# Kernel optimization log

Measured on AMD Instinct MI355X. Metric: run time of the kernel, lower is better.

Reference implementation:

```python
import jax, jax.numpy as jnp
import numpy as np


def rotary_pos_emb(x):
    # x: [..., seq, dim], dim even. Interleaved (GPT-NeoX-style pairwise) rotary.
    dim, seq = x.shape[-1], x.shape[-2]
    ts = jnp.arange(0, dim, 2, dtype=jnp.float32)
    inv_freqs = 10000.0 ** (-ts / dim)
    grid = jnp.arange(seq, dtype=jnp.float32)[:, None] * inv_freqs[None, :]  # [s, dim//2]
    sin = jnp.repeat(jnp.sin(grid), 2, axis=-1).astype(x.dtype)  # [s, dim]
    cos = jnp.repeat(jnp.cos(grid), 2, axis=-1).astype(x.dtype)  # [s, dim]
    x1, x2 = x[..., ::2], x[..., 1::2]
    xs = jnp.stack([-x2, x1], axis=-1).reshape(x.shape)  # interleave (-x2, x1)
    return x * cos + xs * sin


def setup_inputs() -> dict:
    key = jax.random.key(0)
    kx, kq, kk, kv, ko = jax.random.split(key, 5)
    B, S, D = 2, 2048, 1024
    scale = 1.0 / np.sqrt(D)
    x = jax.random.normal(kx, (B, S, D), dtype=jnp.float32)
    mask = jnp.tril(jnp.ones((S, S), dtype=bool))  # causal
    Wq = jax.random.normal(kq, (D, D), dtype=jnp.float32) * scale
    Wk = jax.random.normal(kk, (D, D), dtype=jnp.float32) * scale
    Wv = jax.random.normal(kv, (D, D), dtype=jnp.float32) * scale
    Wo = jax.random.normal(ko, (D, D), dtype=jnp.float32) * scale
    return {"x": x, "mask": mask, "Wq": Wq, "Wk": Wk, "Wv": Wv, "Wo": Wo}


def reference(x, mask, Wq, Wk, Wv, Wo):
    H = 16
    POS_PORTION = 0.5
    B, S, D = x.shape
    K = D // H
    p = int(K * POS_PORTION)

    q = (x @ Wq) / (K ** 0.5)
    q = q.reshape(B, S, H, K).transpose(0, 2, 1, 3)  # b h l k
    q = jnp.concatenate([rotary_pos_emb(q[..., :p]), q[..., p:]], axis=-1)

    k = (x @ Wk).reshape(B, S, H, K).transpose(0, 2, 1, 3)
    k = jnp.concatenate([rotary_pos_emb(k[..., :p]), k[..., p:]], axis=-1)

    v = (x @ Wv).reshape(B, S, H, K).transpose(0, 2, 1, 3)

    logits = jnp.einsum('bhik,bhjk->bhij', q, k)
    # full-precision masked softmax
    l32 = logits.astype(jnp.float32)
    l32 = jnp.where(mask, l32, -1e30)
    a = jax.nn.softmax(l32, axis=-1).astype(logits.dtype)

    y = jnp.einsum('bhij,bhjv->bhiv', a, v)
    y = y.transpose(0, 2, 1, 3).reshape(B, S, D)  # b l (h v)
    return y @ Wo
```

## Files before the change

### kernel.cpp

```cpp
#include <hip/hip_runtime.h>
#include <cstdint>
#include <cstddef>

typedef __bf16 bf16;
typedef __bf16 bf16x8 __attribute__((ext_vector_type(8)));
typedef float  f32x4  __attribute__((ext_vector_type(4)));

#define B_  2
#define S_  2048
#define D_  1024
#define H_  16
#define KH  64

__device__ __forceinline__ void gload_lds16(const bf16* gp, bf16* lds_base) {
    __builtin_amdgcn_global_load_lds(
        (const __attribute__((address_space(1))) unsigned int*)gp,
        (__attribute__((address_space(3))) unsigned int*)lds_base,
        16, 0, 0);
}

__global__ __launch_bounds__(256) void prep(
    const float* __restrict__ x, bf16* __restrict__ xb,
    const float* __restrict__ Wq, const float* __restrict__ Wk,
    const float* __restrict__ Wv, const float* __restrict__ Wo,
    bf16* __restrict__ WqkvT, bf16* __restrict__ WoT)
{
    __shared__ bf16 tl[64][72];
    int z = blockIdx.x;
    if (z < 4096) {
        const int i = (z * 256 + threadIdx.x) * 4;
        const float4 v = *(const float4*)(x + i);
        union { int2 w; bf16 e[4]; } u;
        u.e[0] = (bf16)v.x; u.e[1] = (bf16)v.y;
        u.e[2] = (bf16)v.z; u.e[3] = (bf16)v.w;
        *(int2*)(xb + i) = u.w;
        return;
    }
    z -= 4096;
    const int zx = z & 15, zy = (z >> 4) & 15, zw = z >> 8;
    const float* src = (zw == 0) ? Wq : (zw == 1) ? Wk : (zw == 2) ? Wv : Wo;
    bf16* dst = (zw < 3) ? (WqkvT + (size_t)zw * D_ * D_) : WoT;
    const int r0 = zy * 64;
    const int c0 = zx * 64;
    const int t  = threadIdx.x;
    {
        const int r = t >> 2, cs = (t & 3) * 16;
        const float4* p = (const float4*)(src + (size_t)(r0 + r) * D_ + c0 + cs);
        float4 a0 = p[0], a1 = p[1], a2 = p[2], a3 = p[3];
        tl[cs +  0][r] = (bf16)a0.x; tl[cs +  1][r] = (bf16)a0.y;
        tl[cs +  2][r] = (bf16)a0.z; tl[cs +  3][r] = (bf16)a0.w;
        tl[cs +  4][r] = (bf16)a1.x; tl[cs +  5][r] = (bf16)a1.y;
        tl[cs +  6][r] = (bf16)a1.z; tl[cs +  7][r] = (bf16)a1.w;
        tl[cs +  8][r] = (bf16)a2.x; tl[cs +  9][r] = (bf16)a2.y;
        tl[cs + 10][r] = (bf16)a2.z; tl[cs + 11][r] = (bf16)a2.w;
        tl[cs + 12][r] = (bf16)a3.x; tl[cs + 13][r] = (bf16)a3.y;
        tl[cs + 14][r] = (bf16)a3.z; tl[cs + 15][r] = (bf16)a3.w;
    }
    __syncthreads();
    {
        const int c = t >> 2, rs = (t & 3) * 16;
        union { int4 v[2]; bf16 e[16]; } u;
#pragma unroll
        for (int i = 0; i < 16; ++i) u.e[i] = tl[c][rs + i];
        int4* p = (int4*)(dst + (size_t)(c0 + c) * D_ + r0 + rs);
        p[0] = u.v[0]; p[1] = u.v[1];
    }
}

template <int EPI, int BN>
__global__ __launch_bounds__(256, 2) void gemm_bt(
    const bf16* __restrict__ A, const bf16* __restrict__ BT,
    float* __restrict__ C, int N, int Kd,
    bf16* __restrict__ qp, bf16* __restrict__ kp, bf16* __restrict__ vp)
{
    constexpr int NJF = BN / 32;
    __shared__ bf16 As[128 * 64];
    __shared__ bf16 Bs[BN * 64];
    const int tid  = threadIdx.x;
    const int lane = tid & 63;
    const int wave = tid >> 6;
    const int l15  = lane & 15;
    const int quad = lane >> 4;
    const int m0 = blockIdx.y * 128;
    const int n0 = blockIdx.x * BN;
    const int wm = (wave >> 1) * 64;
    const int wn = (wave & 1) * (BN / 2);

    f32x4 acc[4][NJF];
#pragma unroll
    for (int i = 0; i < 4; ++i)
#pragma unroll
        for (int j = 0; j < NJF; ++j) acc[i][j] = f32x4{0.f, 0.f, 0.f, 0.f};

    for (int k0 = 0; k0 < Kd; k0 += 64) {
        __syncthreads();
#pragma unroll
        for (int c = 0; c < 4; ++c) {
            const int base  = wave * 4096 + c * 1024;
            const int flatb = base + lane * 16;
            const int row   = flatb >> 7;
            const int col   = (flatb & 127) >> 1;
            gload_lds16(A + (size_t)(m0 + row) * Kd + k0 + col, As + (base >> 1));
        }
#pragma unroll
        for (int c = 0; c < NJF; ++c) {
            const int base  = wave * (BN * 32) + c * 1024;
            const int flatb = base + lane * 16;
            const int row   = flatb >> 7;
            const int col   = (flatb & 127) >> 1;
            gload_lds16(BT + (size_t)(n0 + row) * Kd + k0 + col, Bs + (base >> 1));
        }
        __syncthreads();
#pragma unroll
        for (int kk = 0; kk < 64; kk += 32) {
            bf16x8 af[4], bfv[NJF];
#pragma unroll
            for (int i = 0; i < 4; ++i)
                af[i] = *(const bf16x8*)&As[(wm + i * 16 + l15) * 64 + kk + quad * 8];
#pragma unroll
            for (int j = 0; j < NJF; ++j)
                bfv[j] = *(const bf16x8*)&Bs[(wn + j * 16 + l15) * 64 + kk + quad * 8];
#pragma unroll
            for (int i = 0; i < 4; ++i)
#pragma unroll
                for (int j = 0; j < NJF; ++j)
                    acc[i][j] = __builtin_amdgcn_mfma_f32_16x16x32_bf16(
                        af[i], bfv[j], acc[i][j], 0, 0, 0);
        }
    }

#pragma unroll
    for (int i = 0; i < 4; ++i)
#pragma unroll
        for (int j = 0; j < NJF; ++j) {
            const int Rb = m0 + wm + i * 16 + quad * 4;
            const int Cc = n0 + wn + j * 16 + l15;
            if (EPI == 0) {
#pragma unroll
                for (int r = 0; r < 4; ++r)
                    C[(size_t)(Rb + r) * N + Cc] = acc[i][j][r];
            } else {
                const int sec = Cc >> 10, cc = Cc & 1023;
                const int h = cc >> 6, kd = cc & 63;
#pragma unroll
                for (int r = 0; r < 4; ++r) {
                    const int row = Rb + r;
                    const int b = row >> 11, s = row & (S_ - 1);
                    float v = acc[i][j][r];
                    if (sec == 0) {
                        qp[((size_t)(b * H_ + h) * S_ + s) * KH + kd] =
                            (bf16)(v * 0.1803368801111204f);
                    } else if (sec == 1) {
                        if ((kd >> 4) < 2) {
                            const float partner = __shfl_xor(v, 1);
                            const float inv = __builtin_exp2f(
                                -(float)(kd >> 1) * (13.28771237954945f / 16.f));
                            const float ang = (float)s * inv;
                            float sn, cn;
                            __sincosf(ang, &sn, &cn);
                            v = (l15 & 1) ? fmaf(partner, sn, v * cn)
                                          : fmaf(-partner, sn, v * cn);
                        }
                        kp[((size_t)(b * H_ + h) * S_ + s) * KH + kd] = (bf16)v;
                    } else {
                        vp[((size_t)(b * H_ + h) * KH + kd) * S_ + s] = (bf16)v;
                    }
                }
            }
        }
}

__global__ __launch_bounds__(128, 2) void attn(
    const bf16* __restrict__ q, const bf16* __restrict__ k,
    const bf16* __restrict__ vt, bf16* __restrict__ y)
{
    __shared__ bf16 Ks[2][64 * 64];
    __shared__ bf16 VTs[2][64 * 64];
    __shared__ bf16 Ps[2][2][16][64];

    const int z  = blockIdx.x;
    const int v_ = z & 7;
    const int u_ = (z >> 3) & 31;
    const int w_ = z >> 8;
    const int bh = u_;
    const int qt = (w_ == 0) ? v_ : (w_ == 1) ? (15 - v_)
                 : (w_ == 2) ? (16 + v_) : (31 - v_);
    const int b  = bh >> 4, h = bh & 15;
    const int t    = threadIdx.x;
    const int lane = t & 63, wave = t >> 6;
    const int l15  = lane & 15, quad = lane >> 4;
    const int wrow = qt * 64 + wave * 32;

    const bf16* kbh = k  + (size_t)bh * S_ * KH;
    const bf16* vbh = vt + (size_t)bh * KH * S_;

    const int srow = lane >> 3;
    const int sg   = (lane & 7) ^ srow;

    auto stage = [&](int jt, int bb) {
        const int j0 = jt * 64;
#pragma unroll
        for (int i = 0; i < 4; ++i) {
            const int c = wave * 4 + i;
            gload_lds16(kbh + (size_t)(j0 + c * 8 + srow) * KH + sg * 8,
                        &Ks[bb][c * 8 * 64]);
            gload_lds16(vbh + (size_t)(c * 8 + srow) * S_ + j0 + sg * 8,
                        &VTs[bb][c * 8 * 64]);
        }
    };

    bf16x8 qf[2][2];
#pragma unroll
    for (int mi = 0; mi < 2; ++mi) {
        const bf16* qp = q + ((size_t)bh * S_ + wrow + mi * 16 + l15) * KH + quad * 8;
        qf[mi][0] = *(const bf16x8*)qp;
        qf[mi][1] = *(const bf16x8*)(qp + 32);
        const float s = (float)(wrow + mi * 16 + l15);
#pragma unroll
        for (int tt = 0; tt < 4; ++tt) {
            const int i = quad * 4 + tt;
            const float inv = exp2f(-(float)i * (13.28771237954945f / 16.f));
            const float ang = s * inv;
            const float sn = sinf(ang), cn = cosf(ang);
            const float x0 = (float)qf[mi][0][2 * tt], x1 = (float)qf[mi][0][2 * tt + 1];
            qf[mi][0][2 * tt]     = (bf16)(x0 * cn - x1 * sn);
            qf[mi][0][2 * tt + 1] = (bf16)(x1 * cn + x0 * sn);
        }
    }

    bf16x8 ones;
#pragma unroll
    for (int i = 0; i < 8; ++i) ones[i] = (bf16)1.0f;

    f32x4 accO[2][4], lacc[2];
#pragma unroll
    for (int mi = 0; mi < 2; ++mi) {
#pragma unroll
        for (int j = 0; j < 4; ++j) accO[mi][j] = f32x4{0.f, 0.f, 0.f, 0.f};
        lacc[mi] = f32x4{0.f, 0.f, 0.f, 0.f};
    }

    const int nj = qt + 1;
    stage(0, 0);
    for (int jt = 0; jt < nj; ++jt) {
        const int bb = jt & 1;
        __syncthreads();
        if (jt + 1 < nj) stage(jt + 1, bb ^ 1);

        f32x4 accS[2][4];
#pragma unroll
        for (int mi = 0; mi < 2; ++mi)
#pragma unroll
            for (int nb = 0; nb < 4; ++nb) accS[mi][nb] = f32x4{0.f, 0.f, 0.f, 0.f};
#pragma unroll
        for (int c = 0; c < 2; ++c) {
            bf16x8 kf[4];
#pragma unroll
            for (int nb = 0; nb < 4; ++nb)
                kf[nb] = *(const bf16x8*)
                    &Ks[bb][(nb * 16 + l15) * 64 + (((c * 4 + quad) ^ (l15 & 7)) * 8)];
#pragma unroll
            for (int mi = 0; mi < 2; ++mi)
#pragma unroll
                for (int nb = 0; nb < 4; ++nb)
                    accS[mi][nb] = __builtin_amdgcn_mfma_f32_16x16x32_bf16(
                        qf[mi][c], kf[nb], accS[mi][nb], 0, 0, 0);
        }

        if (jt == nj - 1) {
            const int j0 = jt * 64;
#pragma unroll
            for (int mi = 0; mi < 2; ++mi)
#pragma unroll
                for (int nb = 0; nb < 4; ++nb)
#pragma unroll
                    for (int r = 0; r < 4; ++r) {
                        const int qi = wrow + mi * 16 + quad * 4 + r;
                        const int ki = j0 + nb * 16 + l15;
                        if (ki > qi) accS[mi][nb][r] = -1e30f;
                    }
        }

#pragma unroll
        for (int mi = 0; mi < 2; ++mi)
#pragma unroll
            for (int nb = 0; nb < 4; ++nb)
#pragma unroll
                for (int r = 0; r < 4; ++r) {
                    const float p = __builtin_amdgcn_exp2f(accS[mi][nb][r]);
                    const int row = quad * 4 + r;
                    Ps[wave][mi][row][(((nb * 2 + (l15 >> 3)) ^ (row & 7)) * 8) + (l15 & 7)]
                        = (bf16)p;
                }

#pragma unroll
        for (int c = 0; c < 2; ++c) {
            bf16x8 vf[4];
#pragma unroll
            for (int vb = 0; vb < 4; ++vb)
                vf[vb] = *(const bf16x8*)
                    &VTs[bb][(vb * 16 + l15) * 64 + (((c * 4 + quad) ^ (l15 & 7)) * 8)];
            bf16x8 pf[2];
#pragma unroll
            for (int mi = 0; mi < 2; ++mi)
                pf[mi] = *(const bf16x8*)
                    &Ps[wave][mi][l15][((c * 4 + quad) ^ (l15 & 7)) * 8];
#pragma unroll
            for (int mi = 0; mi < 2; ++mi) {
#pragma unroll
                for (int vb = 0; vb < 4; ++vb)
                    accO[mi][vb] = __builtin_amdgcn_mfma_f32_16x16x32_bf16(
                        pf[mi], vf[vb], accO[mi][vb], 0, 0, 0);
                lacc[mi] = __builtin_amdgcn_mfma_f32_16x16x32_bf16(
                    pf[mi], ones, lacc[mi], 0, 0, 0);
            }
        }
    }

#pragma unroll
    for (int mi = 0; mi < 2; ++mi) {
        float rinv[4];
#pragma unroll
        for (int r = 0; r < 4; ++r) rinv[r] = 1.0f / lacc[mi][r];
#pragma unroll
        for (int vb = 0; vb < 4; ++vb)
#pragma unroll
            for (int r = 0; r < 4; ++r) {
                const int row = wrow + mi * 16 + quad * 4 + r;
                const int col = h * KH + vb * 16 + l15;
                y[((size_t)b * S_ + row) * D_ + col] = (bf16)(accO[mi][vb][r] * rinv[r]);
            }
    }
}

extern "C" void kernel_launch(void* const* d_in, const int* in_sizes, int n_in,
                              void* d_out, int out_size, void* d_ws, size_t ws_size,
                              hipStream_t stream)
{
    (void)in_sizes; (void)n_in; (void)out_size; (void)ws_size;
    const float* x  = (const float*)d_in[0];
    const float* Wq = (const float*)d_in[2];
    const float* Wk = (const float*)d_in[3];
    const float* Wv = (const float*)d_in[4];
    const float* Wo = (const float*)d_in[5];
    float* out = (float*)d_out;

    char* ws = (char*)d_ws;
    bf16* WqkvT = (bf16*)(ws + 0);
    bf16* WoT   = (bf16*)(ws + 6291456);
    bf16* xb    = (bf16*)(ws + 8388608);
    bf16* qw    = (bf16*)(ws + 16777216);
    bf16* kw    = (bf16*)(ws + 25165824);
    bf16* vtw   = (bf16*)(ws + 33554432);
    bf16* yw    = (bf16*)(ws + 41943040);

    hipLaunchKernelGGL(prep, dim3(5120), dim3(256), 0, stream,
                       x, xb, Wq, Wk, Wv, Wo, WqkvT, WoT);
    hipLaunchKernelGGL((gemm_bt<1, 128>), dim3(24, 32), dim3(256), 0, stream,
                       xb, WqkvT, (float*)nullptr, 3072, 1024, qw, kw, vtw);
    hipLaunchKernelGGL(attn, dim3(1024), dim3(128), 0, stream, qw, kw, vtw, yw);
    hipLaunchKernelGGL((gemm_bt<0, 64>), dim3(16, 32), dim3(256), 0, stream,
                       yw, WoT, out, 1024, 1024,
                       (bf16*)nullptr, (bf16*)nullptr, (bf16*)nullptr);
}
```

Measured before the change: 204.8 us.

## Keep softmax probabilities in registers by computing transposed S tile

Swaps the MFMA operands for QK^T so each lane holds a column of S matching the A-operand layout of a 16x16x16 bf16 MFMA. The exponentiated probabilities then feed the PV product straight from registers, removing the per-wave LDS round trip for P. PV switches to the K=16 MFMA, which issues twice as many instructions. It also wraps the MFMA blocks in s_setprio to favour matrix issue. The causal mask indices are remapped to the transposed layout.

```diff
diff --git a/kernel.cpp b/kernel.cpp
--- a/kernel.cpp
+++ b/kernel.cpp
@@ -5,6 +5,7 @@
 typedef __bf16 bf16;
 typedef __bf16 bf16x8 __attribute__((ext_vector_type(8)));
 typedef float  f32x4  __attribute__((ext_vector_type(4)));
+typedef short  s16x4  __attribute__((ext_vector_type(4)));
 
 #define B_  2
 #define S_  2048
@@ -176,7 +177,6 @@
 {
     __shared__ bf16 Ks[2][64 * 64];
     __shared__ bf16 VTs[2][64 * 64];
-    __shared__ bf16 Ps[2][2][16][64];
 
     const int z  = blockIdx.x;
     const int v_ = z & 7;
@@ -228,9 +228,9 @@
         }
     }
 
-    bf16x8 ones;
-#pragma unroll
-    for (int i = 0; i < 8; ++i) ones[i] = (bf16)1.0f;
+    s16x4 ones4;
+#pragma unroll
+    for (int i = 0; i < 4; ++i) ones4[i] = (short)0x3F80;
 
     f32x4 accO[2][4], lacc[2];
 #pragma unroll
@@ -259,12 +259,14 @@
             for (int nb = 0; nb < 4; ++nb)
                 kf[nb] = *(const bf16x8*)
                     &Ks[bb][(nb * 16 + l15) * 64 + (((c * 4 + quad) ^ (l15 & 7)) * 8)];
+            __builtin_amdgcn_s_setprio(1);
 #pragma unroll
             for (int mi = 0; mi < 2; ++mi)
 #pragma unroll
                 for (int nb = 0; nb < 4; ++nb)
                     accS[mi][nb] = __builtin_amdgcn_mfma_f32_16x16x32_bf16(
-                        qf[mi][c], kf[nb], accS[mi][nb], 0, 0, 0);
+                        kf[nb], qf[mi][c], accS[mi][nb], 0, 0, 0);
+            __builtin_amdgcn_s_setprio(0);
         }
 
         if (jt == nj - 1) {
@@ -275,45 +277,43 @@
                 for (int nb = 0; nb < 4; ++nb)
 #pragma unroll
                     for (int r = 0; r < 4; ++r) {
-                        const int qi = wrow + mi * 16 + quad * 4 + r;
-                        const int ki = j0 + nb * 16 + l15;
+                        const int qi = wrow + mi * 16 + l15;
+                        const int ki = j0 + nb * 16 + quad * 4 + r;
                         if (ki > qi) accS[mi][nb][r] = -1e30f;
                     }
         }
 
+        s16x4 pf[2][4];
 #pragma unroll
         for (int mi = 0; mi < 2; ++mi)
 #pragma unroll
-            for (int nb = 0; nb < 4; ++nb)
-#pragma unroll
-                for (int r = 0; r < 4; ++r) {
-                    const float p = __builtin_amdgcn_exp2f(accS[mi][nb][r]);
-                    const int row = quad * 4 + r;
-                    Ps[wave][mi][row][(((nb * 2 + (l15 >> 3)) ^ (row & 7)) * 8) + (l15 & 7)]
-                        = (bf16)p;
-                }
-
-#pragma unroll
-        for (int c = 0; c < 2; ++c) {
-            bf16x8 vf[4];
+            for (int nb = 0; nb < 4; ++nb) {
+                union { bf16 hh[4]; s16x4 ss; } u;
+#pragma unroll
+                for (int r = 0; r < 4; ++r)
+                    u.hh[r] = (bf16)__builtin_amdgcn_exp2f(accS[mi][nb][r]);
+                pf[mi][nb] = u.ss;
+            }
+
+#pragma unroll
+        for (int nb = 0; nb < 4; ++nb) {
+            s16x4 vf[4];
 #pragma unroll
             for (int vb = 0; vb < 4; ++vb)
-                vf[vb] = *(const bf16x8*)
-                    &VTs[bb][(vb * 16 + l15) * 64 + (((c * 4 + quad) ^ (l15 & 7)) * 8)];
-            bf16x8 pf[2];
-#pragma unroll
-            for (int mi = 0; mi < 2; ++mi)
-                pf[mi] = *(const bf16x8*)
-                    &Ps[wave][mi][l15][((c * 4 + quad) ^ (l15 & 7)) * 8];
+                vf[vb] = *(const s16x4*)
+                    &VTs[bb][(vb * 16 + l15) * 64 +
+                             (((nb * 2 + (quad >> 1)) ^ (l15 & 7)) * 8) + (quad & 1) * 4];
+            __builtin_amdgcn_s_setprio(1);
 #pragma unroll
             for (int mi = 0; mi < 2; ++mi) {
 #pragma unroll
                 for (int vb = 0; vb < 4; ++vb)
-                    accO[mi][vb] = __builtin_amdgcn_mfma_f32_16x16x32_bf16(
-                        pf[mi], vf[vb], accO[mi][vb], 0, 0, 0);
-                lacc[mi] = __builtin_amdgcn_mfma_f32_16x16x32_bf16(
-                    pf[mi], ones, lacc[mi], 0, 0, 0);
+                    accO[mi][vb] = __builtin_amdgcn_mfma_f32_16x16x16bf16_1k(
+                        pf[mi][nb], vf[vb], accO[mi][vb], 0, 0, 0);
+                lacc[mi] = __builtin_amdgcn_mfma_f32_16x16x16bf16_1k(
+                    pf[mi][nb], ones4, lacc[mi], 0, 0, 0);
             }
+            __builtin_amdgcn_s_setprio(0);
         }
     }
 
```

Result: no change. 204.8 us (+0.0%).
